# Kernel optimization log

Hardware: AMD Instinct MI355X
Metric: run time of the kernel (lower is better)

Reference implementation:

```python
import jax, jax.numpy as jnp
import numpy as np

B_, T_, D_ = 4, 4096, 512
H_, DH_ = 8, 64
N_HASHES, BUCKET = 4, 64
SELF_ATTN_VAL = -5e4  # TOKEN_SELF_ATTN_VALUE from reformer-pytorch


def setup_inputs() -> dict:
    key = jax.random.key(0)
    ks = jax.random.split(key, 12)
    s = 0.02
    return {
        "src": jax.random.normal(ks[0], (B_, T_, D_), jnp.float32),
        "Wqk": jax.random.normal(ks[1], (D_, D_), jnp.float32) * s,
        "Wv": jax.random.normal(ks[2], (D_, D_), jnp.float32) * s,
        "Wout": jax.random.normal(ks[3], (D_, D_), jnp.float32) * s,
        "bout": jnp.zeros((D_,), jnp.float32),
        "W1": jax.random.normal(ks[4], (D_, 2048), jnp.float32) * s,
        "b1": jnp.zeros((2048,), jnp.float32),
        "W2": jax.random.normal(ks[5], (2048, D_), jnp.float32) * s,
        "b2": jnp.zeros((D_,), jnp.float32),
        "gamma": jnp.ones((D_,), jnp.float32),
        "beta": jnp.zeros((D_,), jnp.float32),
        "rotations": jax.random.normal(ks[6], (DH_, N_HASHES, (T_ // BUCKET) // 2), jnp.float32),
    }


def _look_one_back(x):
    # concat each chunk with the previous chunk (wraparound), along the slot axis
    prev = jnp.concatenate([x[:, -1:], x[:, :-1]], axis=1)
    return jnp.concatenate([x, prev], axis=2)


def lsh_attention(qk, v, rotations):
    # qk, v: (B, T, d) with B = batch*heads; shared-QK LSH attention (non-causal,
    # attend_across_buckets=True, allow_duplicate_attention=True, no dropout)
    B, T, d = qk.shape
    n_buckets = T // BUCKET
    # --- hashing ---
    rv = jnp.einsum("btf,fhi->bhti", qk, rotations)          # (B, n_hashes, T, nb/2)
    rv = jnp.concatenate([rv, -rv], axis=-1)                  # (B, n_hashes, T, nb)
    buckets = jnp.argmax(rv, axis=-1)                         # (B, n_hashes, T)
    offsets = (jnp.arange(N_HASHES) * n_buckets)[None, :, None]
    buckets = (buckets + offsets).reshape(B, N_HASHES * T)
    # --- sort by (bucket, position) ---
    ticker = jnp.arange(N_HASHES * T)
    buckets_and_t = buckets * T + (ticker % T)[None, :]
    sticker = jnp.argsort(buckets_and_t, axis=-1)             # (B, n_hashes*T)
    undo_sort = jnp.argsort(sticker, axis=-1)
    st = sticker % T
    sqk = jnp.take_along_axis(qk, st[..., None], axis=1)      # (B, n_hashes*T, d)
    sv = jnp.take_along_axis(v, st[..., None], axis=1)
    # --- chunk ---
    chunks = N_HASHES * n_buckets
    bq_t = st.reshape(B, chunks, BUCKET)
    bqk = sqk.reshape(B, chunks, BUCKET, d)
    bv = sv.reshape(B, chunks, BUCKET, d)
    bq = bqk
    bk = bqk / (jnp.linalg.norm(bqk, axis=-1, keepdims=True) + 1e-6)
    bk = _look_one_back(bk)                                   # (B, chunks, 2*BUCKET, d)
    bv = _look_one_back(bv)
    bkv_t = _look_one_back(bq_t)                              # (B, chunks, 2*BUCKET)
    # --- attention within chunk (+ one look-back chunk) ---
    dots = jnp.einsum("bcie,bcje->bcij", bq, bk) * (d ** -0.5)
    self_mask = bq_t[:, :, :, None] == bkv_t[:, :, None, :]
    dots = jnp.where(self_mask, SELF_ATTN_VAL, dots)
    lse = jax.nn.logsumexp(dots, axis=-1, keepdims=True)
    p = jnp.exp(dots - lse)
    bo = jnp.einsum("bcij,bcje->bcie", p, bv)
    # --- unsort and combine hash rounds ---
    so = bo.reshape(B, N_HASHES * T, d)
    slog = lse.reshape(B, N_HASHES * T)
    o = jnp.take_along_axis(so, undo_sort[..., None], axis=1)
    logits = jnp.take_along_axis(slog, undo_sort, axis=1)
    o = o.reshape(B, N_HASHES, T, d)
    logits = logits.reshape(B, N_HASHES, T, 1)
    probs = jnp.exp(logits - jax.nn.logsumexp(logits, axis=1, keepdims=True))
    return jnp.sum(o * probs, axis=1)                         # (B, T, d)


def _layer(src, Wqk, Wv, Wout, bout, W1, b1, W2, b2, gamma, beta, rotations):
    b, t, dm = src.shape
    qk = src @ Wqk
    v = src @ Wv
    def split(x):
        return x.reshape(b, t, H_, DH_).transpose(0, 2, 1, 3).reshape(b * H_, t, DH_)
    o = lsh_attention(split(qk), split(v), rotations)
    o = o.reshape(b, H_, t, DH_).transpose(0, 2, 1, 3).reshape(b, t, dm)
    attn_out = o @ Wout + bout
    x = src + attn_out                # residual (dropout = identity in eval)
    ffn = jax.nn.relu(x @ W1 + b1) @ W2 + b2
    y = x + ffn
    mu = jnp.mean(y, axis=-1, keepdims=True)
    var = jnp.mean((y - mu) ** 2, axis=-1, keepdims=True)
    return (y - mu) / jnp.sqrt(var + 1e-6) * gamma + beta     # post-norm (norm2)


def reference(src, Wqk, Wv, Wout, bout, W1, b1, W2, b2, gamma, beta, rotations):
    return _layer(src, Wqk, Wv, Wout, bout, W1, b1, W2, b2, gamma, beta, rotations)
```

## Files before the change

kernel.cpp:

```cpp
#include <hip/hip_runtime.h>

#define B_ 4
#define T_ 4096
#define D_ 512
#define H_ 8
#define DH_ 64
#define NH_ 4
#define NB_ 64
#define BH_ (B_*H_)
#define CHUNKS_ (NH_*NB_)
#define NTICK_ (NH_*T_)
#define M_ (B_*T_)
#define FFN_ 2048

typedef __attribute__((ext_vector_type(8))) short bf16x8;
typedef __attribute__((ext_vector_type(4))) float f32x4;

__device__ __forceinline__ unsigned short f2bf(float x) {
  unsigned int u = __float_as_uint(x);
  return (unsigned short)((u + 0x7FFFu + ((u >> 16) & 1u)) >> 16);
}
__device__ __forceinline__ float bf2f(unsigned short s) {
  return __uint_as_float(((unsigned int)s) << 16);
}
__device__ __forceinline__ unsigned int cvt_pk_bf16(float lo, float hi) {
  unsigned int r;
  asm("v_cvt_pk_bf16_f32 %0, %1, %2" : "=v"(r) : "v"(lo), "v"(hi));
  return r;
}

__device__ __forceinline__ void gld_lds16(const void* g, void* l) {
  __builtin_amdgcn_global_load_lds(
      (const __attribute__((address_space(1))) unsigned int*)g,
      (__attribute__((address_space(3))) unsigned int*)l, 16, 0, 0);
}

__device__ __forceinline__ int swf(int row) { return (row ^ (row >> 3)) & 7; }
__device__ __forceinline__ int off64(int row, int k) {
  return row * 64 + (((k >> 3) ^ swf(row)) << 3) + (k & 7);
}
__device__ __forceinline__ int off128(int row, int k) {
  return row * 128 + (((k >> 3) ^ swf(row)) << 3) + (k & 7);
}

template<int BM, int MODE, bool HAS_BIAS, bool RELU, bool HAS_RESID>
__global__ __launch_bounds__(256) void gemm_bf16(
    const unsigned short* __restrict__ A, const unsigned short* __restrict__ BT,
    const float* __restrict__ bias, const unsigned short* __restrict__ resid,
    float* __restrict__ Cf, unsigned short* __restrict__ Cb,
    unsigned short* __restrict__ Cb2, float* __restrict__ invn,
    int M, int N, int K, int lda, int ldbt, int ldr)
{
  constexpr int MI = BM / 32;
  constexpr int ABSZ = (BM + 128) * 64;
  __shared__ __align__(16) unsigned short smem[2 * ABSZ];
  const int tid = threadIdx.x;
  const int lane = tid & 63;
  const int w = tid >> 6;
  const int wm = (w >> 1) * (BM / 2), wn = (w & 1) * 64;
  const int g = lane >> 4, cl = lane & 15;

  const int gx = gridDim.x;
  const int id = blockIdx.x + blockIdx.y * gx;
  const int cpx = (gx * gridDim.y) >> 3;
  const int swz = (id & 7) * cpx + (id >> 3);
  const int m0 = (swz / gx) * BM, n0 = (swz % gx) * 128;

  const bool isv = (MODE == 3) && (n0 >= 512);

  f32x4 acc[MI][4];
#pragma unroll
  for (int i = 0; i < MI; ++i)
#pragma unroll
    for (int j = 0; j < 4; ++j) acc[i][j] = (f32x4){0.f, 0.f, 0.f, 0.f};

  const int srow = tid >> 3;
  const int skc  = (tid & 7) * 8;

#define STAGE(BUF, K0)                                                        \
  do {                                                                        \
    unsigned short* As_ = smem + (BUF) * ABSZ;                                \
    unsigned short* Bs_ = As_ + BM * 64;                                      \
    _Pragma("unroll")                                                         \
    for (int ci = 0; ci < BM / 32; ++ci)                                      \
      gld_lds16(&A[(size_t)(m0 + ci * 32 + srow) * lda + (K0) + skc],         \
                &As_[ci * 2048 + tid * 8]);                                   \
    _Pragma("unroll")                                                         \
    for (int ci = 0; ci < 4; ++ci)                                            \
      gld_lds16(&BT[(size_t)(n0 + ci * 32 + srow) * ldbt + (K0) + skc],       \
                &Bs_[ci * 2048 + tid * 8]);                                   \
  } while (0)

  STAGE(0, 0);
  const int KT = K >> 6;
  for (int kt = 0; kt < KT; ++kt) {
    if (kt + 1 < KT) {
      STAGE((kt + 1) & 1, (kt + 1) * 64);
      asm volatile("s_waitcnt vmcnt(8)" ::: "memory");
    } else {
      asm volatile("s_waitcnt vmcnt(0)" ::: "memory");
    }
    __builtin_amdgcn_s_barrier();
    const unsigned short* As = smem + (kt & 1) * ABSZ;
    const unsigned short* Bs = As + BM * 64;
#pragma unroll
    for (int kk = 0; kk < 64; kk += 32) {
      bf16x8 af[MI], bfr[4];
#pragma unroll
      for (int i = 0; i < MI; ++i)
        af[i] = *(const bf16x8*)&As[(wm + i * 16 + cl) * 64 + kk + g * 8];
#pragma unroll
      for (int j = 0; j < 4; ++j)
        bfr[j] = *(const bf16x8*)&Bs[(wn + j * 16 + cl) * 64 + kk + g * 8];
#pragma unroll
      for (int i = 0; i < MI; ++i)
#pragma unroll
        for (int j = 0; j < 4; ++j)
          acc[i][j] = __builtin_amdgcn_mfma_f32_16x16x32_bf16(af[i], bfr[j], acc[i][j], 0, 0, 0);
    }
    asm volatile("" ::: "memory");
    __builtin_amdgcn_s_barrier();
  }
#undef STAGE

  float bv[4];
  if constexpr (HAS_BIAS) {
#pragma unroll
    for (int j = 0; j < 4; ++j) bv[j] = bias[n0 + wn + j * 16 + cl];
  }
#pragma unroll
  for (int i = 0; i < MI; ++i) {
#pragma unroll
    for (int r = 0; r < 4; ++r) {
      const int lrow = wm + i * 16 + g * 4 + r;
      float v4[4];
      float ss = 0.f;
#pragma unroll
      for (int j = 0; j < 4; ++j) {
        float val = acc[i][j][r];
        if constexpr (HAS_BIAS) val += bv[j];
        if constexpr (RELU) val = fmaxf(val, 0.f);
        v4[j] = val;
        if constexpr (MODE == 3) {
          if (!isv) {
            ss += val * val;
            Cf[(size_t)(m0 + lrow) * 512 + n0 + wn + j * 16 + cl] = val;
          }
        }
      }
      const unsigned int p01 = cvt_pk_bf16(v4[0], v4[1]);
      const unsigned int p23 = cvt_pk_bf16(v4[2], v4[3]);
      const int sw = (lrow & 7) << 3;
      smem[lrow * 128 + ((wn +  0 + cl) ^ sw)] = (unsigned short)p01;
      smem[lrow * 128 + ((wn + 16 + cl) ^ sw)] = (unsigned short)(p01 >> 16);
      smem[lrow * 128 + ((wn + 32 + cl) ^ sw)] = (unsigned short)p23;
      smem[lrow * 128 + ((wn + 48 + cl) ^ sw)] = (unsigned short)(p23 >> 16);
      if constexpr (MODE == 3) {
        if (!isv) {
          ss += __shfl_xor(ss, 1); ss += __shfl_xor(ss, 2);
          ss += __shfl_xor(ss, 4); ss += __shfl_xor(ss, 8);
          if (cl == 0) {
            const int m = m0 + lrow;
            const int bb = m >> 12, t = m & (T_ - 1);
            const int hh = ((n0 + wn) >> 6) & 7;
            invn[((size_t)(bb * 8 + hh)) * T_ + t] = 1.0f / (sqrtf(ss) + 1e-6f);
          }
        }
      }
    }
  }
  __syncthreads();
#pragma unroll
  for (int l = 0; l < BM / 16; ++l) {
    const int idx = tid + l * 256;
    const int row = idx >> 4, c8 = (idx & 15) * 8;
    uint4 u = *(const uint4*)&smem[row * 128 + (c8 ^ ((row & 7) << 3))];
    if constexpr (HAS_RESID) {
      const uint4 rv = *(const uint4*)&resid[(size_t)(m0 + row) * ldr + n0 + c8];
      const unsigned short* sp = (const unsigned short*)&u;
      const unsigned short* rp = (const unsigned short*)&rv;
      float f[8];
#pragma unroll
      for (int e = 0; e < 8; ++e) f[e] = bf2f(sp[e]) + bf2f(rp[e]);
      u.x = cvt_pk_bf16(f[0], f[1]); u.y = cvt_pk_bf16(f[2], f[3]);
      u.z = cvt_pk_bf16(f[4], f[5]); u.w = cvt_pk_bf16(f[6], f[7]);
    }
    if constexpr (MODE == 3) {
      if (isv)
        *(uint4*)&Cb2[(size_t)(m0 + row) * 512 + (n0 - 512) + c8] = u;
      else
        *(uint4*)&Cb[(size_t)(m0 + row) * 512 + n0 + c8] = u;
    } else {
      *(uint4*)&Cb[(size_t)(m0 + row) * N + n0 + c8] = u;
    }
  }
}

__global__ __launch_bounds__(256) void prep_all(
    const float* __restrict__ Wqk, const float* __restrict__ Wv,
    const float* __restrict__ Wout, const float* __restrict__ W1,
    const float* __restrict__ W2, const float* __restrict__ src,
    unsigned short* __restrict__ WqkvT, unsigned short* __restrict__ WoutT,
    unsigned short* __restrict__ W1T, unsigned short* __restrict__ W2T,
    unsigned short* __restrict__ src_b)
{
  __shared__ float tile[32][33];
  int bid = blockIdx.x;
  if (bid >= 2816) {
    const int i = (bid - 2816) * 256 + threadIdx.x;
    const int m = i >> 6, d0 = (i & 63) * 8;
    float x[8];
    *(float4*)&x[0] = *(const float4*)&src[(size_t)m * D_ + d0];
    *(float4*)&x[4] = *(const float4*)&src[(size_t)m * D_ + d0 + 4];
    unsigned short hi[8];
#pragma unroll
    for (int e = 0; e < 8; ++e) hi[e] = f2bf(x[e]);
    *(uint4*)&src_b[(size_t)m * D_ + d0] = *(const uint4*)&hi[0];
    return;
  }
  const float* W; unsigned short* WT; int K, N, bx, by;
  if (bid < 256)        { W = Wqk;  WT = WqkvT; K = 512;  N = 512;
                          bx = bid & 15; by = bid >> 4; }
  else if (bid < 512)   { bid -= 256;  W = Wv; WT = WqkvT + (size_t)512 * 512;
                          K = 512; N = 512;
                          bx = bid & 15; by = bid >> 4; }
  else if (bid < 768)   { bid -= 512;  W = Wout; WT = WoutT; K = 512;  N = 512;
                          bx = bid & 15; by = bid >> 4; }
  else if (bid < 1792)  { bid -= 768;  W = W1;   WT = W1T;   K = 512;  N = 2048;
                          bx = bid & 63; by = bid >> 6; }
  else                  { bid -= 1792; W = W2;   WT = W2T;   K = 2048; N = 512;
                          bx = bid & 15; by = bid >> 4; }
  const int k0 = by * 32, n0 = bx * 32;
  const int tx = threadIdx.x & 31, ty = threadIdx.x >> 5;
#pragma unroll
  for (int r = 0; r < 32; r += 8)
    tile[ty + r][tx] = W[(size_t)(k0 + ty + r) * N + n0 + tx];
  __syncthreads();
#pragma unroll
  for (int r = 0; r < 32; r += 8)
    WT[(size_t)(n0 + ty + r) * K + k0 + tx] = f2bf(tile[tx][ty + r]);
}

__global__ __launch_bounds__(256) void hash_gemm_kernel(
    const float* __restrict__ qk, const float* __restrict__ rot,
    int* __restrict__ buckets)
{
  __shared__ __align__(16) float As[64][136];
  __shared__ __align__(16) float Bs[64][132];
  const int tid = threadIdx.x;
  const int tx = tid & 15, ty = tid >> 4;
  const int t0 = blockIdx.x * 128, bh = blockIdx.y;
  const int b = bh >> 3, hd = bh & 7;

#pragma unroll
  for (int l = 0; l < 8; ++l) {
    const int idx = tid + l * 256;
    const int row = idx >> 4;
    const int kq = (idx & 15) << 2;
    const float4 a = *(const float4*)&qk[((size_t)b * T_ + t0 + row) * D_ + hd * DH_ + kq];
    As[kq + 0][row] = a.x; As[kq + 1][row] = a.y;
    As[kq + 2][row] = a.z; As[kq + 3][row] = a.w;
  }
#pragma unroll
  for (int l = 0; l < 8; ++l) {
    const int idx = tid + l * 256;
    const int kr = idx >> 5;
    const int c4 = (idx & 31) << 2;
    *(float4*)&Bs[kr][c4] = *(const float4*)&rot[kr * 128 + c4];
  }
  __syncthreads();

  float acc[8][8];
#pragma unroll
  for (int i = 0; i < 8; ++i)
#pragma unroll
    for (int j = 0; j < 8; ++j) acc[i][j] = 0.f;

#pragma unroll 4
  for (int kk = 0; kk < 64; ++kk) {
    float a[8], bq[8];
    *(float4*)&a[0]  = *(const float4*)&As[kk][ty * 8];
    *(float4*)&a[4]  = *(const float4*)&As[kk][ty * 8 + 4];
    *(float4*)&bq[0] = *(const float4*)&Bs[kk][tx * 8];
    *(float4*)&bq[4] = *(const float4*)&Bs[kk][tx * 8 + 4];
#pragma unroll
    for (int i = 0; i < 8; ++i)
#pragma unroll
      for (int j = 0; j < 8; ++j)
        acc[i][j] = fmaf(a[i], bq[j], acc[i][j]);
  }
  __syncthreads();

  float* pval = &As[0][0];
  int*   pidx = (int*)&Bs[0][0];
  const int i0 = (tx & 3) * 8;
#pragma unroll
  for (int r = 0; r < 8; ++r) {
    float v = -3.0e38f; int idx = 127;
#pragma unroll
    for (int j = 0; j < 8; ++j) {
      const float p = acc[r][j];
      const int li = i0 + j;
      if (p > v || (p == v && li < idx)) { v = p; idx = li; }
      const float n = -p;
      const int ni = 32 + li;
      if (n > v || (n == v && ni < idx)) { v = n; idx = ni; }
    }
    pval[(ty * 8 + r) * 16 + tx] = v;
    pidx[(ty * 8 + r) * 16 + tx] = idx;
  }
  __syncthreads();

#pragma unroll
  for (int l = 0; l < 2; ++l) {
    const int id = tid + l * 256;
    const int tok = id >> 2, hh = id & 3;
    float v = pval[tok * 16 + hh * 4];
    int idx = pidx[tok * 16 + hh * 4];
#pragma unroll
    for (int e = 1; e < 4; ++e) {
      const float ov = pval[tok * 16 + hh * 4 + e];
      const int oi = pidx[tok * 16 + hh * 4 + e];
      if (ov > v || (ov == v && oi < idx)) { v = ov; idx = oi; }
    }
    buckets[((size_t)bh * NH_ + hh) * T_ + t0 + tok] = idx + hh * NB_;
  }
}

__global__ __launch_bounds__(256) void hist_kernel(
    const int* __restrict__ buckets, int* __restrict__ bstart)
{
  __shared__ int bins[256];
  const int bh = blockIdx.x;
  bins[threadIdx.x] = 0;
  __syncthreads();
  for (int e = threadIdx.x; e < NTICK_; e += 256)
    atomicAdd(&bins[buckets[(size_t)bh * NTICK_ + e]], 1);
  __syncthreads();
  if (threadIdx.x == 0) {
    int run = 0;
    for (int i = 0; i < 256; ++i) { const int c = bins[i]; bins[i] = run; run += c; }
  }
  __syncthreads();
  bstart[bh * 256 + threadIdx.x] = bins[threadIdx.x];
}

__global__ __launch_bounds__(64) void compact_kernel(
    const int* __restrict__ buckets, const int* __restrict__ bstart,
    int* __restrict__ sticker)
{
  const int bucket = blockIdx.x, bh = blockIdx.y;
  const int h = bucket >> 6;
  const int lane = threadIdx.x;
  int base = bstart[bh * 256 + bucket];
  const int* bk = buckets + (size_t)bh * NTICK_ + (size_t)h * T_;
  for (int it = 0; it < 64; ++it) {
    const int t = it * 64 + lane;
    const bool m = (bk[t] == bucket);
    const unsigned long long bal = __ballot(m);
    if (m) {
      const int pos = base + __popcll(bal & ((1ull << lane) - 1ull));
      sticker[(size_t)bh * NTICK_ + pos] = h * T_ + t;
    }
    base += __popcll(bal);
  }
}

__global__ __launch_bounds__(256) void attn_kernel(
    const unsigned short* __restrict__ qkb, const unsigned short* __restrict__ vb,
    const int* __restrict__ sticker, const float* __restrict__ invn,
    unsigned short* __restrict__ orowsb, float* __restrict__ logits)
{
  __shared__ __align__(16) unsigned short Rs[128 * 64];
  __shared__ __align__(16) unsigned short Vs[128 * 64];
  __shared__ int tks[128];
  __shared__ float invs[128];

  const int cx = blockIdx.x;
  const int c = (cx & 7) * 32 + (cx >> 3);
  const int bh = blockIdx.y;
  const int b = bh >> 3, hd = bh & 7;
  const int tid = threadIdx.x;
  const int hr = c >> 6;
  const int w = tid >> 6, lane = tid & 63, g = lane >> 4, cl = lane & 15;

  if (tid < 128) {
    const int sc = (tid < 64) ? c : ((c + CHUNKS_ - 1) & (CHUNKS_ - 1));
    const int tick = sticker[(size_t)bh * NTICK_ + sc * 64 + (tid & 63)];
    const int t = tick & (T_ - 1);
    tks[tid] = t;
    invs[tid] = invn[bh * T_ + t];
  }
  __syncthreads();

  {
    const int sr = lane >> 3, gq = lane & 7;
#pragma unroll
    for (int l = 0; l < 4; ++l) {
      const int row = l * 32 + w * 8 + sr;
      const size_t gb = ((size_t)b * T_ + tks[row]) * D_ + hd * DH_
                      + ((gq ^ swf(row)) << 3);
      const int dst = (l * 32 + w * 8) * 64 + lane * 8;
      gld_lds16(&qkb[gb], &Rs[dst]);
      gld_lds16(&vb[gb],  &Vs[dst]);
    }
  }
  __syncthreads();

  f32x4 sacc[8];
#pragma unroll
  for (int j = 0; j < 8; ++j) sacc[j] = (f32x4){0.f, 0.f, 0.f, 0.f};
  __builtin_amdgcn_s_setprio(1);
#pragma unroll
  for (int kk = 0; kk < 2; ++kk) {
    const bf16x8 aq = *(const bf16x8*)&Rs[off64(w * 16 + cl, kk * 32 + g * 8)];
#pragma unroll
    for (int j = 0; j < 8; ++j) {
      const bf16x8 bk = *(const bf16x8*)&Rs[off64(j * 16 + cl, kk * 32 + g * 8)];
      sacc[j] = __builtin_amdgcn_mfma_f32_16x16x32_bf16(aq, bk, sacc[j], 0, 0, 0);
    }
  }
  __builtin_amdgcn_s_setprio(0);
  const int d0 = (tid & 15) * 4, tg = tid >> 4;
  unsigned int qw[8][2];
#pragma unroll
  for (int e = 0; e < 8; ++e) {
    const uint2 q = *(const uint2*)&Vs[off64(tg * 8 + e, d0)];
    qw[e][0] = q.x; qw[e][1] = q.y;
  }
  __syncthreads();

  {
    unsigned short col[4][8];
#pragma unroll
    for (int e = 0; e < 8; ++e) {
      col[0][e] = (unsigned short)(qw[e][0] & 0xffffu);
      col[1][e] = (unsigned short)(qw[e][0] >> 16);
      col[2][e] = (unsigned short)(qw[e][1] & 0xffffu);
      col[3][e] = (unsigned short)(qw[e][1] >> 16);
    }
#pragma unroll
    for (int dd = 0; dd < 4; ++dd)
      *(uint4*)&Vs[off128(d0 + dd, tg * 8)] = *(const uint4*)&col[dd][0];
  }

  float iv[8]; int tk[8];
#pragma unroll
  for (int j = 0; j < 8; ++j) {
    iv[j] = invs[j * 16 + cl] * 0.125f;
    tk[j] = tks[j * 16 + cl];
  }
  float pinv[4];
#pragma unroll
  for (int r = 0; r < 4; ++r) {
    const int row = w * 16 + g * 4 + r;
    const int tq = tks[row];
    float e8[8];
    float sum = 0.f;
#pragma unroll
    for (int j = 0; j < 8; ++j) {
      float e = __expf(sacc[j][r] * iv[j]);
      if (tq == tk[j]) e = 0.f;
      e8[j] = e;
      sum += e;
    }
    sum += __shfl_xor(sum, 1); sum += __shfl_xor(sum, 2);
    sum += __shfl_xor(sum, 4); sum += __shfl_xor(sum, 8);
    pinv[r] = 1.f / sum;
#pragma unroll
    for (int j = 0; j < 8; j += 2) {
      const unsigned int pk = cvt_pk_bf16(e8[j], e8[j + 1]);
      Rs[off128(row, j * 16 + cl)]       = (unsigned short)pk;
      Rs[off128(row, (j + 1) * 16 + cl)] = (unsigned short)(pk >> 16);
    }
    if (cl == 0)
      logits[((size_t)bh * T_ + tq) * NH_ + hr] = __logf(sum);
  }
  __syncthreads();

  f32x4 oacc[4];
#pragma unroll
  for (int jd = 0; jd < 4; ++jd) oacc[jd] = (f32x4){0.f, 0.f, 0.f, 0.f};
  __builtin_amdgcn_s_setprio(1);
#pragma unroll
  for (int ks = 0; ks < 4; ++ks) {
    const bf16x8 pa = *(const bf16x8*)&Rs[off128(w * 16 + cl, ks * 32 + g * 8)];
#pragma unroll
    for (int jd = 0; jd < 4; ++jd) {
      const bf16x8 vv = *(const bf16x8*)&Vs[off128(jd * 16 + cl, ks * 32 + g * 8)];
      oacc[jd] = __builtin_amdgcn_mfma_f32_16x16x32_bf16(pa, vv, oacc[jd], 0, 0, 0);
    }
  }
  __builtin_amdgcn_s_setprio(0);
  __syncthreads();

#pragma unroll
  for (int r = 0; r < 4; ++r) {
    const int row = w * 16 + g * 4 + r;
    const unsigned int q01 = cvt_pk_bf16(oacc[0][r] * pinv[r], oacc[1][r] * pinv[r]);
    const unsigned int q23 = cvt_pk_bf16(oacc[2][r] * pinv[r], oacc[3][r] * pinv[r]);
    Rs[off64(row,      cl)] = (unsigned short)q01;
    Rs[off64(row, 16 + cl)] = (unsigned short)(q01 >> 16);
    Rs[off64(row, 32 + cl)] = (unsigned short)q23;
    Rs[off64(row, 48 + cl)] = (unsigned short)(q23 >> 16);
  }
  __syncthreads();

#pragma unroll
  for (int l = 0; l < 2; ++l) {
    const int idx = tid + l * 256;
    const int row = idx >> 3, k0 = (idx & 7) * 8;
    *(uint4*)&orowsb[(((size_t)bh * T_ + tks[row]) * NH_ + hr) * DH_ + k0] =
        *(const uint4*)&Rs[off64(row, k0)];
  }
}

__global__ __launch_bounds__(256) void combine_kernel(
    const unsigned short* __restrict__ orowsb, const float* __restrict__ logits,
    unsigned short* __restrict__ ocombb)
{
  const int gid = blockIdx.x * 4 + (threadIdx.x >> 6);
  const int lane = threadIdx.x & 63;
  const int bh = gid >> 12, t = gid & (T_ - 1);
  const int b = bh >> 3, hd = bh & 7;
  const float4 lg = *(const float4*)&logits[((size_t)bh * T_ + t) * NH_];
  const float m = fmaxf(fmaxf(lg.x, lg.y), fmaxf(lg.z, lg.w));
  const float w0 = __expf(lg.x - m), w1 = __expf(lg.y - m);
  const float w2 = __expf(lg.z - m), w3 = __expf(lg.w - m);
  const float inv = 1.f / (w0 + w1 + w2 + w3);
  const size_t rb = ((size_t)bh * T_ + t) * (NH_ * DH_) + lane;
  const float o = w0 * bf2f(orowsb[rb])
                + w1 * bf2f(orowsb[rb + DH_])
                + w2 * bf2f(orowsb[rb + 2 * DH_])
                + w3 * bf2f(orowsb[rb + 3 * DH_]);
  ocombb[((size_t)b * T_ + t) * D_ + hd * DH_ + lane] = f2bf(o * inv);
}

__global__ __launch_bounds__(256) void ln_kernel(
    const unsigned short* __restrict__ yb, const float* __restrict__ gamma,
    const float* __restrict__ beta, float* __restrict__ out)
{
  const int row = blockIdx.x * 4 + (threadIdx.x >> 6);
  const int lane = threadIdx.x & 63;
  const size_t base = (size_t)row * D_ + lane * 8;
  const uint4 u = *(const uint4*)&yb[base];
  const unsigned short* up = (const unsigned short*)&u;
  float x[8];
#pragma unroll
  for (int i = 0; i < 8; ++i) x[i] = bf2f(up[i]);
  float s = 0.f;
#pragma unroll
  for (int i = 0; i < 8; ++i) s += x[i];
#pragma unroll
  for (int m = 32; m >= 1; m >>= 1) s += __shfl_xor(s, m);
  const float mu = s * (1.f / D_);
  float vs = 0.f;
#pragma unroll
  for (int i = 0; i < 8; ++i) { const float d = x[i] - mu; vs += d * d; }
#pragma unroll
  for (int m = 32; m >= 1; m >>= 1) vs += __shfl_xor(vs, m);
  const float rstd = rsqrtf(vs * (1.f / D_) + 1e-6f);
  float gm[8], bt[8];
  *(float4*)&gm[0] = *(const float4*)&gamma[lane * 8];
  *(float4*)&gm[4] = *(const float4*)&gamma[lane * 8 + 4];
  *(float4*)&bt[0] = *(const float4*)&beta[lane * 8];
  *(float4*)&bt[4] = *(const float4*)&beta[lane * 8 + 4];
  float o[8];
#pragma unroll
  for (int i = 0; i < 8; ++i) o[i] = (x[i] - mu) * rstd * gm[i] + bt[i];
  *(float4*)&out[base]     = make_float4(o[0], o[1], o[2], o[3]);
  *(float4*)&out[base + 4] = make_float4(o[4], o[5], o[6], o[7]);
}

extern "C" void kernel_launch(void* const* d_in, const int* in_sizes, int n_in,
                              void* d_out, int out_size, void* d_ws, size_t ws_size,
                              hipStream_t stream) {
  (void)in_sizes; (void)n_in; (void)out_size; (void)ws_size;
  const float* src   = (const float*)d_in[0];
  const float* Wqk   = (const float*)d_in[1];
  const float* Wv    = (const float*)d_in[2];
  const float* Wout  = (const float*)d_in[3];
  const float* bout  = (const float*)d_in[4];
  const float* W1    = (const float*)d_in[5];
  const float* b1    = (const float*)d_in[6];
  const float* W2    = (const float*)d_in[7];
  const float* b2    = (const float*)d_in[8];
  const float* gamma = (const float*)d_in[9];
  const float* beta  = (const float*)d_in[10];
  const float* rot   = (const float*)d_in[11];
  float* out = (float*)d_out;

  char* ws = (char*)d_ws;
  const size_t MB = 1024 * 1024;
  float*          qk      = (float*)(ws);
  unsigned short* src_b   = (unsigned short*)(ws + 32 * MB);
  unsigned short* v_b     = (unsigned short*)(ws + 48 * MB);
  unsigned short* orows_b = (unsigned short*)(ws + 64 * MB);
  unsigned short* qk_b    = (unsigned short*)(ws + 128 * MB);
  char* p = ws + 144 * MB;
  float* logits  = (float*)p; p += (size_t)BH_ * T_ * NH_ * 4;
  int*   buckets = (int*)p;   p += (size_t)BH_ * NH_ * T_ * 4;
  int*   sticker = (int*)p;   p += (size_t)BH_ * NTICK_ * 4;
  int*   bstart  = (int*)p;   p += (size_t)BH_ * 256 * 4;
  float* invn    = (float*)p; p += (size_t)BH_ * T_ * 4;
  unsigned short* WqkvT = (unsigned short*)p; p += (size_t)1024 * 512 * 2;
  unsigned short* WoutT = (unsigned short*)p; p += (size_t)D_ * D_ * 2;
  unsigned short* W1T   = (unsigned short*)p; p += (size_t)FFN_ * D_ * 2;
  unsigned short* W2T   = (unsigned short*)p; p += (size_t)D_ * FFN_ * 2;

  unsigned short* ocomb_b  = qk_b;
  unsigned short* x_b      = v_b;
  unsigned short* hidden_b = orows_b;
  unsigned short* ybuf_b   = (unsigned short*)ws;

  prep_all<<<2816 + M_ * D_ / 8 / 256, 256, 0, stream>>>(
      Wqk, Wv, Wout, W1, W2, src, WqkvT, WoutT, W1T, W2T, src_b);

  gemm_bf16<128, 3, false, false, false>
      <<<dim3(1024 / 128, M_ / 128), 256, 0, stream>>>(
      src_b, WqkvT, nullptr, nullptr, qk, qk_b, v_b, invn,
      M_, 1024, D_, D_, D_, 0);
  hash_gemm_kernel<<<dim3(T_ / 128, BH_), 256, 0, stream>>>(qk, rot, buckets);
  hist_kernel<<<BH_, 256, 0, stream>>>(buckets, bstart);
  compact_kernel<<<dim3(256, BH_), 64, 0, stream>>>(buckets, bstart, sticker);
  attn_kernel<<<dim3(CHUNKS_, BH_), 256, 0, stream>>>(
      qk_b, v_b, sticker, invn, orows_b, logits);
  combine_kernel<<<BH_ * T_ / 4, 256, 0, stream>>>(orows_b, logits, ocomb_b);
  gemm_bf16<128, 1, true, false, true>
      <<<dim3(D_ / 128, M_ / 128), 256, 0, stream>>>(
      ocomb_b, WoutT, bout, src_b, nullptr, x_b, nullptr, nullptr,
      M_, D_, D_, D_, D_, D_);
  gemm_bf16<128, 1, true, true, false>
      <<<dim3(FFN_ / 128, M_ / 128), 256, 0, stream>>>(
      x_b, W1T, b1, nullptr, nullptr, hidden_b, nullptr, nullptr,
      M_, FFN_, D_, D_, D_, 0);
  gemm_bf16<128, 1, true, false, true>
      <<<dim3(D_ / 128, M_ / 128), 256, 0, stream>>>(
      hidden_b, W2T, b2, x_b, nullptr, ybuf_b, nullptr, nullptr,
      M_, D_, FFN_, FFN_, FFN_, D_);
  ln_kernel<<<M_ / 4, 256, 0, stream>>>(ybuf_b, gamma, beta, out);
}
```

Baseline: 332.6 us.

## Add 256x256-tile 512-thread GEMM kernel for FFN up-projection with ReLU

```diff
diff --git a/kernel.cpp b/kernel.cpp
--- a/kernel.cpp
+++ b/kernel.cpp
@@ -41,6 +41,120 @@
 }
 __device__ __forceinline__ int off128(int row, int k) {
   return row * 128 + (((k >> 3) ^ swf(row)) << 3) + (k & 7);
+}
+
+__global__ __launch_bounds__(512) void gemm256_relu(
+    const unsigned short* __restrict__ A, const unsigned short* __restrict__ BT,
+    const float* __restrict__ bias, unsigned short* __restrict__ Cb,
+    int M, int N, int K)
+{
+  constexpr int ABSZ = 32768;
+  __shared__ __align__(16) unsigned short smem[2 * ABSZ];
+  const int tid = threadIdx.x;
+  const int lane = tid & 63, w = tid >> 6;
+  const int wm = (w >> 2) * 128, wn = (w & 3) * 64;
+  const int g = lane >> 4, cl = lane & 15;
+
+  const int gx = gridDim.x;
+  const int id = blockIdx.x + blockIdx.y * gx;
+  const int cpx = (gx * gridDim.y) >> 3;
+  const int swz = (id & 7) * cpx + (id >> 3);
+  const int m0 = (swz / gx) * 256, n0 = (swz % gx) * 256;
+
+  f32x4 acc[8][4];
+#pragma unroll
+  for (int i = 0; i < 8; ++i)
+#pragma unroll
+    for (int j = 0; j < 4; ++j) acc[i][j] = (f32x4){0.f, 0.f, 0.f, 0.f};
+
+#define STG256(BUF, KB, P)                                                    \
+  do {                                                                        \
+    const bool isA_ = (P) < 2;                                                \
+    const int half_ = (P) & 1;                                                \
+    const unsigned short* Mp_ = isA_ ? A : BT;                                \
+    const int gb_ = isA_ ? m0 : n0;                                           \
+    const int ro_ = isA_ ? 0 : 16384;                                         \
+    _Pragma("unroll")                                                         \
+    for (int c2 = 0; c2 < 2; ++c2) {                                          \
+      const int r_ = half_ * 128 + w * 16 + c2 * 8 + (lane >> 3);             \
+      const int kg_ = (lane & 7) ^ swf(r_);                                   \
+      gld_lds16(&Mp_[(size_t)(gb_ + r_) * K + (KB) + kg_ * 8],                \
+                &smem[(BUF) * ABSZ + ro_ +                                    \
+                      (half_ * 128 + w * 16 + c2 * 8) * 64 + lane * 8]);      \
+    }                                                                         \
+  } while (0)
+
+#pragma unroll
+  for (int p = 0; p < 4; ++p) STG256(0, 0, p);
+
+  const int KT = K >> 6;
+  for (int kt = 0; kt < KT; ++kt) {
+    const int cur = kt & 1;
+    const unsigned short* As = smem + cur * ABSZ;
+    const unsigned short* Bs = As + 16384;
+#pragma unroll
+    for (int p = 0; p < 4; ++p) {
+      if (kt + 1 < KT) STG256(cur ^ 1, (kt + 1) * 64, p);
+      if (p == 0) {
+        if (kt + 1 < KT) asm volatile("s_waitcnt vmcnt(2)" ::: "memory");
+        else             asm volatile("s_waitcnt vmcnt(0)" ::: "memory");
+        __builtin_amdgcn_s_barrier();
+      }
+      const int rq = wm + (p >> 1) * 64, cq = wn + (p & 1) * 32;
+      bf16x8 af[4][2], bfr[2][2];
+#pragma unroll
+      for (int i = 0; i < 4; ++i)
+#pragma unroll
+        for (int kk = 0; kk < 2; ++kk)
+          af[i][kk] = *(const bf16x8*)&As[off64(rq + i * 16 + cl, kk * 32 + g * 8)];
+#pragma unroll
+      for (int j = 0; j < 2; ++j)
+#pragma unroll
+        for (int kk = 0; kk < 2; ++kk)
+          bfr[j][kk] = *(const bf16x8*)&Bs[off64(cq + j * 16 + cl, kk * 32 + g * 8)];
+      __builtin_amdgcn_s_setprio(1);
+#pragma unroll
+      for (int kk = 0; kk < 2; ++kk)
+#pragma unroll
+        for (int i = 0; i < 4; ++i)
+#pragma unroll
+          for (int j = 0; j < 2; ++j)
+            acc[(p >> 1) * 4 + i][(p & 1) * 2 + j] =
+                __builtin_amdgcn_mfma_f32_16x16x32_bf16(
+                    af[i][kk], bfr[j][kk], acc[(p >> 1) * 4 + i][(p & 1) * 2 + j], 0, 0, 0);
+      __builtin_amdgcn_s_setprio(0);
+      if (p == 3) __builtin_amdgcn_s_barrier();
+    }
+  }
+#undef STG256
+
+  float bv[4];
+#pragma unroll
+  for (int j4 = 0; j4 < 4; ++j4) bv[j4] = bias[n0 + wn + j4 * 16 + cl];
+#pragma unroll
+  for (int i = 0; i < 8; ++i) {
+#pragma unroll
+    for (int r = 0; r < 4; ++r) {
+      const int lrow = wm + i * 16 + g * 4 + r;
+      const int sw = (lrow & 7) << 3;
+#pragma unroll
+      for (int j4 = 0; j4 < 4; j4 += 2) {
+        const float v0 = fmaxf(acc[i][j4][r] + bv[j4], 0.f);
+        const float v1 = fmaxf(acc[i][j4 + 1][r] + bv[j4 + 1], 0.f);
+        const unsigned int pk = cvt_pk_bf16(v0, v1);
+        smem[lrow * 256 + ((wn + j4 * 16 + cl) ^ sw)]       = (unsigned short)pk;
+        smem[lrow * 256 + ((wn + (j4 + 1) * 16 + cl) ^ sw)] = (unsigned short)(pk >> 16);
+      }
+    }
+  }
+  __syncthreads();
+#pragma unroll
+  for (int l = 0; l < 16; ++l) {
+    const int idx = tid + l * 512;
+    const int row = idx >> 5, c8 = (idx & 31) * 8;
+    const uint4 u = *(const uint4*)&smem[row * 256 + (c8 ^ ((row & 7) << 3))];
+    *(uint4*)&Cb[(size_t)(m0 + row) * N + n0 + c8] = u;
+  }
 }
 
 template<int BM, int MODE, bool HAS_BIAS, bool RELU, bool HAS_RESID>
@@ -630,10 +744,8 @@
       <<<dim3(D_ / 128, M_ / 128), 256, 0, stream>>>(
       ocomb_b, WoutT, bout, src_b, nullptr, x_b, nullptr, nullptr,
       M_, D_, D_, D_, D_, D_);
-  gemm_bf16<128, 1, true, true, false>
-      <<<dim3(FFN_ / 128, M_ / 128), 256, 0, stream>>>(
-      x_b, W1T, b1, nullptr, nullptr, hidden_b, nullptr, nullptr,
-      M_, FFN_, D_, D_, D_, 0);
+  gemm256_relu<<<dim3(FFN_ / 256, M_ / 256), 512, 0, stream>>>(
+      x_b, W1T, b1, hidden_b, M_, FFN_, D_);
   gemm_bf16<128, 1, true, false, true>
       <<<dim3(D_ / 128, M_ / 128), 256, 0, stream>>>(
       hidden_b, W2T, b2, x_b, nullptr, ybuf_b, nullptr, nullptr,
```

Measured after the change: 325.6 us. 1.02x faster.
